# Kernel optimization log

Measured on AMD Instinct MI355X. Metric: run time of the kernel, lower is better.

The kernel has to match this reference:

```python
import jax, jax.numpy as jnp
import numpy as np

SCALE = 64.0
MARGIN = 0.35
EPS = 1e-12  # torch F.normalize eps


def _l2norm(a, axis):
    n = jnp.sqrt(jnp.sum(a * a, axis=axis, keepdims=True))
    return a / jnp.maximum(n, EPS)


def setup_inputs() -> dict:
    key = jax.random.key(0)
    k1, k2, k3 = jax.random.split(key, 3)
    B, D, C = 512, 512, 100000
    x = jax.random.normal(k1, (B, D), dtype=jnp.float32)
    gt = jax.random.randint(k2, (B,), 0, C, dtype=jnp.int64)
    # kaiming_normal_ on [C, D]: std = sqrt(2 / fan_in) with fan_in = D
    wt = jax.random.normal(k3, (C, D), dtype=jnp.float32) * np.sqrt(2.0 / D)
    return {"x": x, "gt": gt, "wt": wt}


def reference(x, gt, wt):
    wt_norm = _l2norm(wt, axis=1)          # [C, D]
    x_norm = _l2norm(x, axis=1)            # [B, D]
    cos = jnp.einsum("bd,cd->bc", x_norm, wt_norm)  # [B, C]
    # margin only at target index (avoids materializing one-hot)
    b = jnp.arange(x.shape[0])
    margin_score = cos.at[b, gt].add(-MARGIN)
    logits = SCALE * margin_score
    logp = jax.nn.log_softmax(logits, axis=-1)
    nll = -logp[b, gt]
    return jnp.mean(nll)
```

## Files before the change

### kernel.cpp

```cpp
#include <hip/hip_runtime.h>
#include <hip/hip_bf16.h>

#define DIM 512
#define BATCH 512
#define CCLS 100000
#define BM 128
#define BN 128
#define NT 782

typedef __attribute__((ext_vector_type(8))) short bf16x8;
typedef __attribute__((ext_vector_type(4))) float f32x4;

__device__ __forceinline__ unsigned short f2bf(float f) {
  union { float f; unsigned int u; } v; v.f = f;
  unsigned int u = v.u;
  return (unsigned short)((u + 0x7fffu + ((u >> 16) & 1u)) >> 16);
}

__device__ __forceinline__ void async_copy16(const unsigned short* g, unsigned short* l) {
  __builtin_amdgcn_global_load_lds((const __attribute__((address_space(1))) void*)g,
                                   (__attribute__((address_space(3))) void*)l, 16, 0, 0);
}

__global__ __launch_bounds__(256) void rownorm_bf16(const float* __restrict__ in,
                                                    unsigned short* __restrict__ out,
                                                    int R) {
  int wave = threadIdx.x >> 6;
  int lane = threadIdx.x & 63;
  int row = blockIdx.x * 4 + wave;
  if (row >= R) return;
  const float4* src = (const float4*)(in + (size_t)row * DIM);
  float4 v0 = src[lane];
  float4 v1 = src[lane + 64];
  float ss = v0.x*v0.x + v0.y*v0.y + v0.z*v0.z + v0.w*v0.w
           + v1.x*v1.x + v1.y*v1.y + v1.z*v1.z + v1.w*v1.w;
  #pragma unroll
  for (int off = 32; off > 0; off >>= 1) ss += __shfl_xor(ss, off, 64);
  float r = 1.0f / fmaxf(sqrtf(ss), 1e-12f);
  ushort4 o0, o1;
  o0.x = f2bf(v0.x * r); o0.y = f2bf(v0.y * r); o0.z = f2bf(v0.z * r); o0.w = f2bf(v0.w * r);
  o1.x = f2bf(v1.x * r); o1.y = f2bf(v1.y * r); o1.z = f2bf(v1.z * r); o1.w = f2bf(v1.w * r);
  ushort4* dst = (ushort4*)(out + (size_t)row * DIM);
  dst[lane]      = o0;
  dst[lane + 64] = o1;
}

__global__ __launch_bounds__(256) void cosface_gemm(
    const unsigned short* __restrict__ xn,
    const unsigned short* __restrict__ wn,
    const int* __restrict__ gt,
    float* __restrict__ partial,
    float* __restrict__ tgt) {
  __shared__ unsigned short lds_a[BM * 64];
  __shared__ unsigned short lds_b[BN * 64];
  __shared__ float lds_rowsum[BM];
  __shared__ int lds_gt[BM];

  const int tid = threadIdx.x;
  const int lane = tid & 63;
  const int w = tid >> 6;
  const int wm = w >> 1;
  const int wn_ = w & 1;
  const int mt = blockIdx.x;
  const int nt = blockIdx.y;

  const unsigned short* ga[4];
  const unsigned short* gb[4];
  #pragma unroll
  for (int j = 0; j < 4; ++j) {
    int c = j * 256 + w * 64 + lane;
    int m = c >> 3;
    int qg = (c & 7) ^ (m & 7);
    int rowA = mt * BM + m;
    int rowB = nt * BN + m;
    if (rowB >= CCLS) rowB = CCLS - 1;
    ga[j] = xn + (size_t)rowA * DIM + qg * 8;
    gb[j] = wn + (size_t)rowB * DIM + qg * 8;
  }

  f32x4 acc[4][4];
  #pragma unroll
  for (int i = 0; i < 4; ++i)
    #pragma unroll
    for (int j = 0; j < 4; ++j)
      acc[i][j] = (f32x4){0.f, 0.f, 0.f, 0.f};

  const int quad = lane >> 4;
  const int l15 = lane & 15;

  for (int kk = 0; kk < 8; ++kk) {
    #pragma unroll
    for (int j = 0; j < 4; ++j) {
      async_copy16(ga[j] + kk * 64, &lds_a[(j * 256 + w * 64) * 8]);
      async_copy16(gb[j] + kk * 64, &lds_b[(j * 256 + w * 64) * 8]);
    }
    __syncthreads();
    #pragma unroll
    for (int s = 0; s < 2; ++s) {
      bf16x8 af[4], bf[4];
      int q = s * 4 + quad;
      #pragma unroll
      for (int i = 0; i < 4; ++i) {
        int ml = wm * 64 + i * 16 + l15;
        af[i] = *(const bf16x8*)&lds_a[ml * 64 + ((q ^ (ml & 7)) * 8)];
        int nl = wn_ * 64 + i * 16 + l15;
        bf[i] = *(const bf16x8*)&lds_b[nl * 64 + ((q ^ (nl & 7)) * 8)];
      }
      #pragma unroll
      for (int i = 0; i < 4; ++i)
        #pragma unroll
        for (int j = 0; j < 4; ++j)
          acc[i][j] = __builtin_amdgcn_mfma_f32_16x16x32_bf16(af[i], bf[j], acc[i][j], 0, 0, 0);
    }
    __syncthreads();
  }

  if (tid < BM) {
    lds_rowsum[tid] = 0.f;
    lds_gt[tid] = gt[mt * BM + tid];
  }
  __syncthreads();

  #pragma unroll
  for (int i = 0; i < 4; ++i) {
    #pragma unroll
    for (int reg = 0; reg < 4; ++reg) {
      int m_loc = wm * 64 + i * 16 + quad * 4 + reg;
      int m_g = mt * BM + m_loc;
      int gtm = lds_gt[m_loc];
      float s = 0.f;
      #pragma unroll
      for (int j = 0; j < 4; ++j) {
        int n_g = nt * BN + wn_ * 64 + j * 16 + l15;
        float logit = 64.f * acc[i][j][reg];
        if (n_g == gtm) {
          logit -= 64.f * 0.35f;
          tgt[m_g] = logit;
        }
        if (n_g < CCLS) s += __expf(logit - 64.f);
      }
      #pragma unroll
      for (int off = 1; off < 16; off <<= 1) s += __shfl_xor(s, off, 64);
      if (l15 == 0) atomicAdd(&lds_rowsum[m_loc], s);
    }
  }
  __syncthreads();
  if (tid < BM) partial[(size_t)nt * BATCH + mt * BM + tid] = lds_rowsum[tid];
}

__global__ __launch_bounds__(512) void finalize(const float* __restrict__ partial,
                                                const float* __restrict__ tgt,
                                                float* __restrict__ out) {
  __shared__ float red[BATCH];
  int m = threadIdx.x;
  float s = 0.f;
  for (int t = 0; t < NT; ++t) s += partial[(size_t)t * BATCH + m];
  float nll = (logf(s) + 64.f) - tgt[m];
  red[m] = nll;
  __syncthreads();
  for (int k = 256; k > 0; k >>= 1) {
    if (m < k) red[m] += red[m + k];
    __syncthreads();
  }
  if (m == 0) out[0] = red[0] * (1.0f / BATCH);
}

extern "C" void kernel_launch(void* const* d_in, const int* in_sizes, int n_in,
                              void* d_out, int out_size, void* d_ws, size_t ws_size,
                              hipStream_t stream) {
  const float* x  = (const float*)d_in[0];
  const int*   gt = (const int*)d_in[1];
  const float* wt = (const float*)d_in[2];
  float* out = (float*)d_out;

  char* ws = (char*)d_ws;
  unsigned short* wn = (unsigned short*)ws;
  unsigned short* xn = (unsigned short*)(ws + 102400000);
  float* partial     = (float*)(ws + 102400000 + 524288);
  float* tgt         = (float*)(ws + 102400000 + 524288 + 1601536);

  rownorm_bf16<<<CCLS / 4, 256, 0, stream>>>(wt, wn, CCLS);
  rownorm_bf16<<<BATCH / 4, 256, 0, stream>>>(x, xn, BATCH);
  cosface_gemm<<<dim3(4, NT), 256, 0, stream>>>(xn, wn, gt, partial, tgt);
  finalize<<<1, BATCH, 0, stream>>>(partial, tgt, out);
}
```

Baseline: 415.7 us.

## Merge normalization launches, parallelize final reduction, and add occupancy hint to GEMM

The two row-normalization launches are merged into a single kernel, saving one launch. The single-block finalize, which had 512 threads each serially summing 782 partials, is split into a 512-block per-row reduction kernel and a small mean kernel. Partials are now stored row-major so each row's partials are contiguous for the new reduction. The GEMM also loads gt into LDS before the K loop, removing one barrier, and gets a launch_bounds occupancy hint of 4, which may constrain register allocation.

```diff
diff --git a/kernel.cpp b/kernel.cpp
--- a/kernel.cpp
+++ b/kernel.cpp
@@ -22,13 +22,18 @@
                                    (__attribute__((address_space(3))) void*)l, 16, 0, 0);
 }
 
-__global__ __launch_bounds__(256) void rownorm_bf16(const float* __restrict__ in,
-                                                    unsigned short* __restrict__ out,
-                                                    int R) {
+__global__ __launch_bounds__(256) void rownorm_all(const float* __restrict__ wt,
+                                                   const float* __restrict__ x,
+                                                   unsigned short* __restrict__ wn,
+                                                   unsigned short* __restrict__ xn) {
   int wave = threadIdx.x >> 6;
   int lane = threadIdx.x & 63;
-  int row = blockIdx.x * 4 + wave;
-  if (row >= R) return;
+  int row4 = blockIdx.x * 4 + wave;
+  const float* in;
+  unsigned short* out;
+  int row;
+  if (row4 < CCLS) { in = wt; out = wn; row = row4; }
+  else             { in = x;  out = xn; row = row4 - CCLS; }
   const float4* src = (const float4*)(in + (size_t)row * DIM);
   float4 v0 = src[lane];
   float4 v1 = src[lane + 64];
@@ -45,7 +50,7 @@
   dst[lane + 64] = o1;
 }
 
-__global__ __launch_bounds__(256) void cosface_gemm(
+__global__ __launch_bounds__(256, 4) void cosface_gemm(
     const unsigned short* __restrict__ xn,
     const unsigned short* __restrict__ wn,
     const int* __restrict__ gt,
@@ -64,6 +69,11 @@
   const int mt = blockIdx.x;
   const int nt = blockIdx.y;
 
+  if (tid < BM) {
+    lds_rowsum[tid] = 0.f;
+    lds_gt[tid] = gt[mt * BM + tid];
+  }
+
   const unsigned short* ga[4];
   const unsigned short* gb[4];
   #pragma unroll
@@ -115,12 +125,6 @@
     __syncthreads();
   }
 
-  if (tid < BM) {
-    lds_rowsum[tid] = 0.f;
-    lds_gt[tid] = gt[mt * BM + tid];
-  }
-  __syncthreads();
-
   #pragma unroll
   for (int i = 0; i < 4; ++i) {
     #pragma unroll
@@ -145,18 +149,28 @@
     }
   }
   __syncthreads();
-  if (tid < BM) partial[(size_t)nt * BATCH + mt * BM + tid] = lds_rowsum[tid];
-}
-
-__global__ __launch_bounds__(512) void finalize(const float* __restrict__ partial,
-                                                const float* __restrict__ tgt,
-                                                float* __restrict__ out) {
+  if (tid < BM)
+    partial[(size_t)(mt * BM + tid) * NT + nt] = lds_rowsum[tid];
+}
+
+__global__ __launch_bounds__(64) void nll_rows(const float* __restrict__ partial,
+                                               const float* __restrict__ tgt,
+                                               float* __restrict__ nll) {
+  int m = blockIdx.x;
+  int lane = threadIdx.x;
+  const float* row = partial + (size_t)m * NT;
+  float s = 0.f;
+  for (int t = lane; t < NT; t += 64) s += row[t];
+  #pragma unroll
+  for (int off = 32; off > 0; off >>= 1) s += __shfl_xor(s, off, 64);
+  if (lane == 0) nll[m] = (logf(s) + 64.f) - tgt[m];
+}
+
+__global__ __launch_bounds__(512) void reduce_mean(const float* __restrict__ nll,
+                                                   float* __restrict__ out) {
   __shared__ float red[BATCH];
   int m = threadIdx.x;
-  float s = 0.f;
-  for (int t = 0; t < NT; ++t) s += partial[(size_t)t * BATCH + m];
-  float nll = (logf(s) + 64.f) - tgt[m];
-  red[m] = nll;
+  red[m] = nll[m];
   __syncthreads();
   for (int k = 256; k > 0; k >>= 1) {
     if (m < k) red[m] += red[m + k];
@@ -178,9 +192,10 @@
   unsigned short* xn = (unsigned short*)(ws + 102400000);
   float* partial     = (float*)(ws + 102400000 + 524288);
   float* tgt         = (float*)(ws + 102400000 + 524288 + 1601536);
-
-  rownorm_bf16<<<CCLS / 4, 256, 0, stream>>>(wt, wn, CCLS);
-  rownorm_bf16<<<BATCH / 4, 256, 0, stream>>>(x, xn, BATCH);
+  float* nll         = (float*)(ws + 102400000 + 524288 + 1601536 + 2048);
+
+  rownorm_all<<<(CCLS + BATCH) / 4, 256, 0, stream>>>(wt, x, wn, xn);
   cosface_gemm<<<dim3(4, NT), 256, 0, stream>>>(xn, wn, gt, partial, tgt);
-  finalize<<<1, BATCH, 0, stream>>>(partial, tgt, out);
-}
+  nll_rows<<<BATCH, 64, 0, stream>>>(partial, tgt, nll);
+  reduce_mean<<<1, BATCH, 0, stream>>>(nll, out);
+}
```

New measurement: 365.8 us. 12.0% less time.
